# Optimization experiments

Measured on AMD Instinct MI355X. Metric: run time of the kernel, lower is better.

## Reference

```python
import jax, jax.numpy as jnp
import numpy as np

B = 512; D = 128; NL = 16; LAYERS = 4; H = 4; HD = D // H
MAX_D = 128; MAX_E = 512
N_DRUG = 25600; N_ENZ = 153600


def setup_inputs() -> dict:
    key = jax.random.key(0)
    ks = jax.random.split(key, 40)
    it = iter(range(40))
    def nrm(shape, scale=0.02):
        return jax.random.normal(ks[next(it)], shape, jnp.float32) * scale
    inp = {}
    inp["drug_k"] = jax.random.normal(ks[next(it)], (N_DRUG, D), jnp.float32)
    inp["drug_v"] = jax.random.normal(ks[next(it)], (N_DRUG, D), jnp.float32)
    inp["enzyme_k"] = jax.random.normal(ks[next(it)], (N_ENZ, D), jnp.float32)
    inp["enzyme_v"] = jax.random.normal(ks[next(it)], (N_ENZ, D), jnp.float32)
    inp["drug_batch"] = jnp.sort(jax.random.randint(ks[next(it)], (N_DRUG,), 0, B))
    inp["enzyme_batch"] = jnp.sort(jax.random.randint(ks[next(it)], (N_ENZ,), 0, B))
    inp["latents"] = nrm((1, NL, D), 1.0)
    inp["wq_d"] = nrm((LAYERS, D, D)); inp["bq_d"] = jnp.zeros((LAYERS, D), jnp.float32)
    inp["wq_e"] = nrm((LAYERS, D, D)); inp["bq_e"] = jnp.zeros((LAYERS, D), jnp.float32)
    inp["mha_d_w"] = nrm((LAYERS, 3 * D, D)); inp["mha_d_b"] = jnp.zeros((LAYERS, 3 * D), jnp.float32)
    inp["mha_d_ow"] = nrm((LAYERS, D, D)); inp["mha_d_ob"] = jnp.zeros((LAYERS, D), jnp.float32)
    inp["mha_e_w"] = nrm((LAYERS, 3 * D, D)); inp["mha_e_b"] = jnp.zeros((LAYERS, 3 * D), jnp.float32)
    inp["mha_e_ow"] = nrm((LAYERS, D, D)); inp["mha_e_ob"] = jnp.zeros((LAYERS, D), jnp.float32)
    inp["ln1_g"] = jnp.ones((LAYERS, D), jnp.float32); inp["ln1_b"] = jnp.zeros((LAYERS, D), jnp.float32)
    inp["ln2_g"] = jnp.ones((LAYERS, D), jnp.float32); inp["ln2_b"] = jnp.zeros((LAYERS, D), jnp.float32)
    inp["ffn_w1"] = nrm((LAYERS, 2 * D, D)); inp["ffn_b1"] = jnp.zeros((LAYERS, 2 * D), jnp.float32)
    inp["ffn_w2"] = nrm((LAYERS, D, 2 * D)); inp["ffn_b2"] = jnp.zeros((LAYERS, D), jnp.float32)
    inp["head_w1"] = nrm((D, D * NL)); inp["head_b1"] = jnp.zeros((D,), jnp.float32)
    inp["head_w2"] = nrm((1, D)); inp["head_b2"] = jnp.zeros((1,), jnp.float32)
    return inp


def to_dense(x, batch, max_len):
    # PyG to_dense_batch: ragged [N, D] -> padded [B, max_len, D] + bool mask
    ones = jnp.ones_like(batch)
    counts = jax.ops.segment_sum(ones, batch, num_segments=B)
    starts = jnp.concatenate([jnp.zeros((1,), counts.dtype), jnp.cumsum(counts)[:-1]])
    pos = jnp.arange(batch.shape[0]) - starts[batch]
    dense = jnp.zeros((B, max_len, x.shape[-1]), x.dtype).at[batch, pos].set(x)
    mask = jnp.zeros((B, max_len), bool).at[batch, pos].set(True)
    return dense, mask


def layer_norm(x, g, b):
    m = x.mean(-1, keepdims=True)
    v = ((x - m) ** 2).mean(-1, keepdims=True)
    return (x - m) / jnp.sqrt(v + 1e-5) * g + b


def mha(q, k, v, mask, w, b, ow, ob):
    # torch nn.MultiheadAttention (batch_first) with key_padding_mask (~mask = ignore)
    wq, wk, wv = w[:D], w[D:2 * D], w[2 * D:]
    bq, bk, bv = b[:D], b[D:2 * D], b[2 * D:]
    qh = (q @ wq.T + bq).reshape(q.shape[0], -1, H, HD)
    kh = (k @ wk.T + bk).reshape(k.shape[0], -1, H, HD)
    vh = (v @ wv.T + bv).reshape(v.shape[0], -1, H, HD)
    s = jnp.einsum('bqhd,bkhd->bhqk', qh, kh) / jnp.sqrt(jnp.float32(HD))
    s = jnp.where(mask[:, None, None, :], s, jnp.float32(-1e9))
    a = jax.nn.softmax(s, axis=-1)
    o = jnp.einsum('bhqk,bkhd->bqhd', a, vh).reshape(q.shape[0], -1, D)
    return o @ ow.T + ob


def forward_impl(drug_k, drug_v, enzyme_k, enzyme_v, latents,
                 wq_d, bq_d, wq_e, bq_e,
                 mha_d_w, mha_d_b, mha_d_ow, mha_d_ob,
                 mha_e_w, mha_e_b, mha_e_ow, mha_e_ob,
                 ln1_g, ln1_b, ln2_g, ln2_b,
                 ffn_w1, ffn_b1, ffn_w2, ffn_b2,
                 head_w1, head_b1, head_w2, head_b2,
                 drug_batch, enzyme_batch):
    dK, dM = to_dense(drug_k, drug_batch, MAX_D)
    dV, _ = to_dense(drug_v, drug_batch, MAX_D)
    eK, eM = to_dense(enzyme_k, enzyme_batch, MAX_E)
    eV, _ = to_dense(enzyme_v, enzyme_batch, MAX_E)
    lat = jnp.broadcast_to(latents, (B, NL, D))
    for l in range(LAYERS):
        nl = layer_norm(lat, ln1_g[l], ln1_b[l])
        q_d = nl @ wq_d[l].T + bq_d[l]
        q_e = nl @ wq_e[l].T + bq_e[l]
        ad = mha(q_d, dK, dV, dM, mha_d_w[l], mha_d_b[l], mha_d_ow[l], mha_d_ob[l])
        ae = mha(q_e, eK, eV, eM, mha_e_w[l], mha_e_b[l], mha_e_ow[l], mha_e_ob[l])
        lat = lat + ad + ae
        h = layer_norm(lat, ln2_g[l], ln2_b[l])
        h = jax.nn.relu(h @ ffn_w1[l].T + ffn_b1[l]) @ ffn_w2[l].T + ffn_b2[l]
        lat = lat + h
    flat = lat.reshape(B, NL * D)
    h = jax.nn.relu(flat @ head_w1.T + head_b1)
    return jax.nn.softplus(h @ head_w2.T + head_b2)[:, 0]


def reference(drug_k, drug_v, enzyme_k, enzyme_v, drug_batch, enzyme_batch, latents,
              wq_d, bq_d, wq_e, bq_e,
              mha_d_w, mha_d_b, mha_d_ow, mha_d_ob,
              mha_e_w, mha_e_b, mha_e_ow, mha_e_ob,
              ln1_g, ln1_b, ln2_g, ln2_b,
              ffn_w1, ffn_b1, ffn_w2, ffn_b2,
              head_w1, head_b1, head_w2, head_b2):
    return forward_impl(drug_k, drug_v, enzyme_k, enzyme_v, latents,
                        wq_d, bq_d, wq_e, bq_e,
                        mha_d_w, mha_d_b, mha_d_ow, mha_d_ob,
                        mha_e_w, mha_e_b, mha_e_ow, mha_e_ob,
                        ln1_g, ln1_b, ln2_g, ln2_b,
                        ffn_w1, ffn_b1, ffn_w2, ffn_b2,
                        head_w1, head_b1, head_w2, head_b2,
                        drug_batch, enzyme_batch)
```

## Files before the change

kernel.cpp:

```cpp
#include <hip/hip_runtime.h>
#include <math.h>

#define NL 16
#define DD 128

typedef __attribute__((ext_vector_type(8))) short short8;
typedef __attribute__((ext_vector_type(4))) float floatx4;

union U8 { short8 v; unsigned short s[8]; };

__device__ __forceinline__ unsigned short f2bf(float x) {
  union { float f; unsigned u; } v; v.f = x; return (unsigned short)(v.u >> 16);
}
__device__ __forceinline__ float bf2f(unsigned short s) {
  union { unsigned u; float f; } v; v.u = ((unsigned)s) << 16; return v.f;
}

__global__ void seg_kernel(const int* __restrict__ db, int nd,
                           const int* __restrict__ eb, int ne,
                           int* __restrict__ seg) {
  const int* arr = (blockIdx.x == 0) ? db : eb;
  int n = (blockIdx.x == 0) ? nd : ne;
  int* start = seg + blockIdx.x * 1024;
  int* cnt = start + 512;
  int b = threadIdx.x;
  if (b < 512) {
    int lo = 0, hi = n;
    while (lo < hi) { int mid = (lo + hi) >> 1; if (arr[mid] < b) lo = mid + 1; else hi = mid; }
    int s = lo;
    lo = s; hi = n;
    while (lo < hi) { int mid = (lo + hi) >> 1; if (arr[mid] < b + 1) lo = mid + 1; else hi = mid; }
    start[b] = s; cnt[b] = lo - s;
  }
}

__global__ void init_lat_kernel(const float* __restrict__ latents, float* __restrict__ lat) {
  int i = blockIdx.x * blockDim.x + threadIdx.x;
  ((float4*)lat)[i] = ((const float4*)latents)[i & 511];
}

__global__ void cvtw_kernel(const float* __restrict__ mw_d, const float* __restrict__ ow_d,
                            const float* __restrict__ mw_e, const float* __restrict__ ow_e,
                            const float* __restrict__ w1, const float* __restrict__ w2,
                            unsigned short* __restrict__ Wbf) {
  int l = blockIdx.x >> 7, blk = blockIdx.x & 127;
  int idx = blk * 1024 + threadIdx.x * 4;
  const float* src; int off;
  if (idx < 16384)      { src = mw_d + (size_t)l * 49152 + 32768; off = idx; }
  else if (idx < 32768) { src = ow_d + (size_t)l * 16384; off = idx - 16384; }
  else if (idx < 49152) { src = mw_e + (size_t)l * 49152 + 32768; off = idx - 32768; }
  else if (idx < 65536) { src = ow_e + (size_t)l * 16384; off = idx - 49152; }
  else if (idx < 98304) { src = w1 + (size_t)l * 32768; off = idx - 65536; }
  else                  { src = w2 + (size_t)l * 32768; off = idx - 98304; }
  float4 v = *(const float4*)(src + off);
  ushort4 o = { f2bf(v.x), f2bf(v.y), f2bf(v.z), f2bf(v.w) };
  *(ushort4*)(Wbf + (size_t)l * 131072 + idx) = o;
}

__global__ void cvth_kernel(const float* __restrict__ w1, unsigned short* __restrict__ dst) {
  int i = blockIdx.x * blockDim.x + threadIdx.x;
  float4 v = ((const float4*)w1)[i];
  ushort4 o = { f2bf(v.x), f2bf(v.y), f2bf(v.z), f2bf(v.w) };
  ((ushort4*)dst)[i] = o;
}

__global__ __launch_bounds__(256) void fold_kernel(
    const float* __restrict__ wq_d, const float* __restrict__ bq_d,
    const float* __restrict__ wq_e, const float* __restrict__ bq_e,
    const float* __restrict__ mw_d, const float* __restrict__ mb_d,
    const float* __restrict__ mw_e, const float* __restrict__ mb_e,
    float* __restrict__ Wqf, float* __restrict__ bqf) {
  __shared__ __align__(16) float sMW[2048];
  const int pb = blockIdx.x >> 3, rg = blockIdx.x & 7;
  const int l = pb >> 1, p = pb & 1;
  const float* wq = (p == 0 ? wq_d : wq_e) + (size_t)l * 16384;
  const float* bq = (p == 0 ? bq_d : bq_e) + l * 128;
  const float* mw = (p == 0 ? mw_d : mw_e) + (size_t)l * 49152;
  const float* mb = (p == 0 ? mb_d : mb_e) + l * 384;
  const float scale = 0.17677669529663687f;
  const int tid = threadIdx.x;
  {
    const float4* src = (const float4*)(mw + rg * 2048);
    ((float4*)sMW)[tid] = src[tid];
    ((float4*)sMW)[tid + 256] = src[tid + 256];
  }
  __syncthreads();
  const int j = tid & 127, ih = tid >> 7;
  float acc[8];
#pragma unroll
  for (int r = 0; r < 8; ++r) acc[r] = 0.f;
#pragma unroll 4
  for (int k = 0; k < 128; ++k) {
    float wv = wq[k * 128 + j];
#pragma unroll
    for (int r = 0; r < 8; ++r) acc[r] += sMW[(ih * 8 + r) * 128 + k] * wv;
  }
  float* W = Wqf + (size_t)pb * 16384 + (rg * 16 + ih * 8) * 128 + j;
#pragma unroll
  for (int r = 0; r < 8; ++r) W[r * 128] = acc[r] * scale;
  if (rg == 0 && tid < 128) {
    float s = 0.f;
    const float* mr = mw + tid * 128;
    for (int k = 0; k < 128; ++k) s += mr[k] * bq[k];
    bqf[pb * 128 + tid] = (s + mb[tid]) * scale;
  }
}

__global__ __launch_bounds__(256) void wt_kernel(
    const float* __restrict__ Wqf, const float* __restrict__ bqf,
    const float* __restrict__ mw_d, const float* __restrict__ mw_e,
    unsigned short* __restrict__ WtB, float* __restrict__ bt) {
  const int l = blockIdx.x >> 3, p = (blockIdx.x >> 2) & 1, h = blockIdx.x & 3;
  const float* wqf = Wqf + (size_t)(l * 2 + p) * 16384 + (h * 32) * 128;
  const float* wk  = (p == 0 ? mw_d : mw_e) + (size_t)l * 49152 + 16384 + (h * 32) * 128;
  const float* bqv = bqf + (l * 2 + p) * 128 + h * 32;
  __shared__ __align__(16) float sWq[4096];
  __shared__ __align__(16) float sWk[4096];
  __shared__ float sBq[32];
  const int tid = threadIdx.x;
  for (int i = tid; i < 1024; i += 256) {
    ((float4*)sWq)[i] = ((const float4*)wqf)[i];
    ((float4*)sWk)[i] = ((const float4*)wk)[i];
  }
  if (tid < 32) sBq[tid] = bqv[tid];
  __syncthreads();
  const int d = tid & 127, kh = tid >> 7;
  const int n = p * 512 + h * 128 + d;
  const int tn = n >> 4, m = n & 15;
  unsigned short* outl = WtB + (size_t)l * 131072;
#pragma unroll
  for (int kc = 0; kc < 4; ++kc) {
    int k0 = kh * 64 + kc * 16;
    float acc[16];
#pragma unroll
    for (int kk = 0; kk < 16; ++kk) acc[kk] = 0.f;
    for (int j = 0; j < 32; ++j) {
      float wkd = sWk[j * 128 + d];
#pragma unroll
      for (int kk = 0; kk < 16; ++kk) acc[kk] += sWq[j * 128 + k0 + kk] * wkd;
    }
#pragma unroll
    for (int kk = 0; kk < 16; ++kk) {
      int k = k0 + kk;
      int c = k >> 5, quad = (k >> 3) & 3, j8 = k & 7;
      int lane = quad * 16 + m;
      outl[(((size_t)tn * 4 + c) * 64 + lane) * 8 + j8] = f2bf(acc[kk]);
    }
  }
  if (kh == 0) {
    float a = 0.f;
    for (int j = 0; j < 32; ++j) a += sBq[j] * sWk[j * 128 + d];
    bt[l * 1024 + n] = a;
  }
}

__global__ __launch_bounds__(256) void qtilde_kernel(
    const float* __restrict__ lat,
    const float* __restrict__ lng, const float* __restrict__ lnb,
    const unsigned short* __restrict__ WtBl, const float* __restrict__ btl,
    unsigned short* __restrict__ Qt) {
  __shared__ __align__(16) unsigned short sNL[16 * 136];
  const int tid = threadIdx.x;
  const int b = blockIdx.x;
  {
    int q = tid >> 4, li = tid & 15, d0 = li * 8;
    const float* xr = lat + ((size_t)b * NL + q) * DD + d0;
    float x[8];
    *(float4*)(x) = *(const float4*)(xr);
    *(float4*)(x + 4) = *(const float4*)(xr + 4);
    float s1 = 0.f, s2 = 0.f;
#pragma unroll
    for (int j = 0; j < 8; ++j) { s1 += x[j]; s2 += x[j] * x[j]; }
#pragma unroll
    for (int o = 1; o < 16; o <<= 1) { s1 += __shfl_xor(s1, o); s2 += __shfl_xor(s2, o); }
    float mean = s1 * (1.f / 128.f);
    float var = s2 * (1.f / 128.f) - mean * mean;
    float rstd = rsqrtf(var + 1e-5f);
    float y[8];
#pragma unroll
    for (int j = 0; j < 8; ++j)
      y[j] = (x[j] - mean) * rstd * lng[d0 + j] + lnb[d0 + j];
    ushort4 o0 = { f2bf(y[0]), f2bf(y[1]), f2bf(y[2]), f2bf(y[3]) };
    ushort4 o1 = { f2bf(y[4]), f2bf(y[5]), f2bf(y[6]), f2bf(y[7]) };
    *(ushort4*)(sNL + q * 136 + d0) = o0;
    *(ushort4*)(sNL + q * 136 + d0 + 4) = o1;
  }
  __syncthreads();
  const int lane = tid & 63, w = tid >> 6, m = lane & 15, quad = lane >> 4;
  short8 aF[4];
  {
    const unsigned short* arow = sNL + m * 136 + quad * 8;
#pragma unroll
    for (int c = 0; c < 4; ++c) aF[c] = *(const short8*)(arow + c * 32);
  }
  unsigned short* qtb = Qt + (size_t)b * 16384;
#pragma unroll
  for (int t = 0; t < 16; ++t) {
    int tn = w * 16 + t;
    floatx4 acc = (floatx4){0.f, 0.f, 0.f, 0.f};
#pragma unroll
    for (int c = 0; c < 4; ++c) {
      short8 bF = *(const short8*)(WtBl + (((size_t)tn * 4 + c) * 64 + lane) * 8);
      acc = __builtin_amdgcn_mfma_f32_16x16x32_bf16(aF[c], bF, acc, 0, 0, 0);
    }
    int n = tn * 16 + m;
    float bb = btl[n];
    int p = n >> 9, h = (n >> 7) & 3, d = n & 127;
    unsigned short* op = qtb + (p * 64 + h * 16) * 128 + d;
#pragma unroll
    for (int r = 0; r < 4; ++r) op[(quad * 4 + r) * 128] = f2bf(acc[r] + bb);
  }
}

__global__ __launch_bounds__(256, 4) void attn3_kernel(
    const float* __restrict__ Kd32, const float* __restrict__ Vd32,
    const float* __restrict__ Ke32, const float* __restrict__ Ve32,
    unsigned short* __restrict__ Kd, unsigned short* __restrict__ Vd,
    unsigned short* __restrict__ Ke, unsigned short* __restrict__ Ve,
    const int* __restrict__ seg,
    const unsigned short* __restrict__ Qt, int qstride, int cvt,
    unsigned short* __restrict__ part_d, float* __restrict__ l_d,
    unsigned short* __restrict__ part_e, float* __restrict__ l_e) {
  __shared__ __align__(16) unsigned short sK[32 * 136];
  __shared__ __align__(16) unsigned short sV[128 * 40];
  __shared__ __align__(16) unsigned short sP[64 * 40];
  const int tid = threadIdx.x;
  const int bi = blockIdx.x;

  const float* Kp32; const float* Vp32;
  unsigned short* KpB; unsigned short* VpB;
  const unsigned short* qt;
  unsigned short* part; float* lpart;
  int len, st;
  if (bi < 2048) {
    int b = bi >> 2, sp = bi & 3;
    int n = seg[1536 + b]; if (n > 512) n = 512;
    int chunk = (n + 3) >> 2;
    int begin = sp * chunk;
    len = n - begin; if (len > chunk) len = chunk; if (len < 0) len = 0;
    st = seg[1024 + b] + begin;
    Kp32 = Ke32; Vp32 = Ve32; KpB = Ke; VpB = Ve;
    qt = Qt + (size_t)b * qstride + 8192;
    part = part_e + (size_t)bi * 8192;
    lpart = l_e + (size_t)bi * 64;
  } else {
    int b = bi - 2048;
    int n = seg[512 + b]; if (n > 128) n = 128;
    len = n;
    st = seg[b];
    Kp32 = Kd32; Vp32 = Vd32; KpB = Kd; VpB = Vd;
    qt = Qt + (size_t)b * qstride;
    part = part_d + (size_t)b * 8192;
    lpart = l_d + (size_t)b * 64;
  }

  const int lane = tid & 63;
  const int w = tid >> 6;
  const int m = lane & 15;
  const int quad = lane >> 4;

  short8 qA[4];
  {
    const unsigned short* qrow = qt + (size_t)(w * 16 + m) * 128 + quad * 8;
#pragma unroll
    for (int c = 0; c < 4; ++c) qA[c] = *(const short8*)(qrow + c * 32);
  }

  floatx4 oA[8];
#pragma unroll
  for (int i = 0; i < 8; ++i) oA[i] = (floatx4){0.f, 0.f, 0.f, 0.f};
  float lp[4] = {0.f, 0.f, 0.f, 0.f};

  short8 rK[2], rV[2];
  const short8 z8 = {0, 0, 0, 0, 0, 0, 0, 0};
  auto load_tile = [&](int t0) {
    int nv = len - t0; if (nv > 32) nv = 32;
    if (cvt) {
#pragma unroll
      for (int it = 0; it < 2; ++it) {
        int f = tid + it * 256;
        int tok = f >> 4, d8 = f & 15;
        if (tok < nv) {
          size_t g = (size_t)(st + t0 + tok) * 128 + d8 * 8;
          const float* s = Kp32 + g;
          float4 a = *(const float4*)s, c = *(const float4*)(s + 4);
          U8 u;
          u.s[0]=f2bf(a.x); u.s[1]=f2bf(a.y); u.s[2]=f2bf(a.z); u.s[3]=f2bf(a.w);
          u.s[4]=f2bf(c.x); u.s[5]=f2bf(c.y); u.s[6]=f2bf(c.z); u.s[7]=f2bf(c.w);
          rK[it] = u.v;
          *(short8*)(KpB + g) = u.v;
        } else rK[it] = z8;
      }
#pragma unroll
      for (int it = 0; it < 2; ++it) {
        int f = tid + it * 256;
        int tok = f >> 4, d8 = f & 15;
        if (tok < nv) {
          size_t g = (size_t)(st + t0 + tok) * 128 + d8 * 8;
          const float* s = Vp32 + g;
          float4 a = *(const float4*)s, c = *(const float4*)(s + 4);
          U8 u;
          u.s[0]=f2bf(a.x); u.s[1]=f2bf(a.y); u.s[2]=f2bf(a.z); u.s[3]=f2bf(a.w);
          u.s[4]=f2bf(c.x); u.s[5]=f2bf(c.y); u.s[6]=f2bf(c.z); u.s[7]=f2bf(c.w);
          rV[it] = u.v;
          *(short8*)(VpB + g) = u.v;
        } else rV[it] = z8;
      }
    } else {
#pragma unroll
      for (int it = 0; it < 2; ++it) {
        int f = tid + it * 256;
        int tok = f >> 4, d8 = f & 15;
        size_t g = (size_t)(st + t0 + tok) * 128 + d8 * 8;
        rK[it] = (tok < nv) ? *(const short8*)(KpB + g) : z8;
        rV[it] = (tok < nv) ? *(const short8*)(VpB + g) : z8;
      }
    }
  };
  auto store_tile = [&]() {
#pragma unroll
    for (int it = 0; it < 2; ++it) {
      int f = tid + it * 256;
      int tok = f >> 4, d8 = f & 15;
      *(short8*)(sK + tok * 136 + d8 * 8) = rK[it];
      U8 u; u.v = rV[it];
#pragma unroll
      for (int i = 0; i < 8; ++i) {
        int j = (i + d8) & 7;
        sV[(d8 * 8 + j) * 40 + tok] = u.s[j];
      }
    }
  };

  if (len > 0) load_tile(0);
  for (int t0 = 0; t0 < len; t0 += 32) {
    __syncthreads();
    store_tile();
    __syncthreads();
    if (t0 + 32 < len) load_tile(t0 + 32);
    int nv = len - t0; if (nv > 32) nv = 32;
    floatx4 sS[2];
    sS[0] = (floatx4){0.f, 0.f, 0.f, 0.f};
    sS[1] = (floatx4){0.f, 0.f, 0.f, 0.f};
#pragma unroll
    for (int g = 0; g < 2; ++g)
#pragma unroll
      for (int c = 0; c < 4; ++c) {
        short8 kB = *(const short8*)(sK + (g * 16 + m) * 136 + c * 32 + quad * 8);
        sS[g] = __builtin_amdgcn_mfma_f32_16x16x32_bf16(qA[c], kB, sS[g], 0, 0, 0);
      }
#pragma unroll
    for (int g = 0; g < 2; ++g) {
      bool valid = (g * 16 + m) < nv;
#pragma unroll
      for (int r = 0; r < 4; ++r) {
        float p = valid ? __expf(sS[g][r]) : 0.f;
        lp[r] += p;
        sP[(w * 16 + quad * 4 + r) * 40 + g * 16 + m] = f2bf(p);
      }
    }
    short8 pA = *(const short8*)(sP + (w * 16 + m) * 40 + quad * 8);
#pragma unroll
    for (int dg = 0; dg < 8; ++dg) {
      short8 vB = *(const short8*)(sV + (dg * 16 + m) * 40 + quad * 8);
      oA[dg] = __builtin_amdgcn_mfma_f32_16x16x32_bf16(pA, vB, oA[dg], 0, 0, 0);
    }
  }

#pragma unroll
  for (int r = 0; r < 4; ++r) {
    float v = lp[r];
    v += __shfl_xor(v, 1); v += __shfl_xor(v, 2);
    v += __shfl_xor(v, 4); v += __shfl_xor(v, 8);
    lp[r] = v;
  }
  if (m == 0) {
#pragma unroll
    for (int r = 0; r < 4; ++r)
      lpart[w * 16 + quad * 4 + r] = lp[r];
  }
#pragma unroll
  for (int dg = 0; dg < 8; ++dg)
#pragma unroll
    for (int r = 0; r < 4; ++r)
      part[(w * 16 + quad * 4 + r) * 128 + dg * 16 + m] = f2bf(oA[dg][r]);
}

__global__ __launch_bounds__(256) void post_kernel(
    const unsigned short* __restrict__ pd, const float* __restrict__ ldv,
    const unsigned short* __restrict__ pe, const float* __restrict__ lev,
    const unsigned short* __restrict__ Wl,
    const float* __restrict__ bv_d, const float* __restrict__ ob_d,
    const float* __restrict__ bv_e, const float* __restrict__ ob_e,
    const float* __restrict__ ln2g, const float* __restrict__ ln2b,
    const float* __restrict__ b1, const float* __restrict__ b2,
    float* __restrict__ lat,
    const float* __restrict__ lng1, const float* __restrict__ lnb1,
    const unsigned short* __restrict__ WtB_next, const float* __restrict__ bt_next,
    unsigned short* __restrict__ Qt) {
  const unsigned short* wv_d = Wl;
  const unsigned short* ow_d = Wl + 16384;
  const unsigned short* wv_e = Wl + 32768;
  const unsigned short* ow_e = Wl + 49152;
  const unsigned short* w1   = Wl + 65536;
  const unsigned short* w2   = Wl + 98304;

  __shared__ __align__(16) unsigned short sX[64 * 136];
  __shared__ __align__(16) unsigned short sVH[16 * 136];
  __shared__ __align__(16) unsigned short sF[16 * 264];
  __shared__ __align__(16) float sAcc[16 * 132];
  __shared__ float sLd[64], sLe[64];

  const int tid = threadIdx.x;
  const int b = blockIdx.x;
  const int lane = tid & 63;
  const int w = tid >> 6;
  const int m = lane & 15;
  const int quad = lane >> 4;

  if (tid < 64) {
    float v = ldv[(size_t)b * 64 + tid];
    sLd[tid] = (v > 0.f) ? 1.f / v : 0.f;
  } else if (tid < 128) {
    int r = tid - 64;
    float v = lev[((size_t)b * 4 + 0) * 64 + r] + lev[((size_t)b * 4 + 1) * 64 + r]
            + lev[((size_t)b * 4 + 2) * 64 + r] + lev[((size_t)b * 4 + 3) * 64 + r];
    sLe[r] = (v > 0.f) ? 1.f / v : 0.f;
  }
  __syncthreads();
  {
    const ushort4* src = (const ushort4*)(pd + (size_t)b * 8192);
#pragma unroll
    for (int it = 0; it < 8; ++it) {
      int f = tid + it * 256;
      int row = f >> 5, d = (f & 31) * 4;
      ushort4 u = src[f];
      float sc = sLd[row];
      ushort4 o = { f2bf(bf2f(u.x) * sc), f2bf(bf2f(u.y) * sc),
                    f2bf(bf2f(u.z) * sc), f2bf(bf2f(u.w) * sc) };
      *(ushort4*)(sX + row * 136 + d) = o;
    }
  }
  __syncthreads();
  {
    short8 aF[4];
    const unsigned short* arow = sX + (w * 16 + m) * 136 + quad * 8;
#pragma unroll
    for (int c = 0; c < 4; ++c) aF[c] = *(const short8*)(arow + c * 32);
#pragma unroll
    for (int t = 0; t < 2; ++t) {
      int n = w * 32 + t * 16 + m;
      floatx4 acc = (floatx4){0.f, 0.f, 0.f, 0.f};
      const unsigned short* brow = wv_d + n * 128 + quad * 8;
#pragma unroll
      for (int c = 0; c < 4; ++c)
        acc = __builtin_amdgcn_mfma_f32_16x16x32_bf16(aF[c], *(const short8*)(brow + c * 32), acc, 0, 0, 0);
      float bb = bv_d[n];
#pragma unroll
      for (int r = 0; r < 4; ++r) sVH[(quad * 4 + r) * 136 + n] = f2bf(acc[r] + bb);
    }
  }
  __syncthreads();
  {
    short8 aF[4];
    const unsigned short* arow = sVH + m * 136 + quad * 8;
#pragma unroll
    for (int c = 0; c < 4; ++c) aF[c] = *(const short8*)(arow + c * 32);
#pragma unroll
    for (int t = 0; t < 2; ++t) {
      int n = w * 32 + t * 16 + m;
      floatx4 acc = (floatx4){0.f, 0.f, 0.f, 0.f};
      const unsigned short* brow = ow_d + n * 128 + quad * 8;
#pragma unroll
      for (int c = 0; c < 4; ++c)
        acc = __builtin_amdgcn_mfma_f32_16x16x32_bf16(aF[c], *(const short8*)(brow + c * 32), acc, 0, 0, 0);
      float bb = ob_d[n];
#pragma unroll
      for (int r = 0; r < 4; ++r) {
        int q = quad * 4 + r;
        sAcc[q * 132 + n] = lat[(size_t)b * 2048 + q * 128 + n] + acc[r] + bb;
      }
    }
  }
  __syncthreads();
  {
    const ushort4* s0 = (const ushort4*)(pe + ((size_t)b * 4 + 0) * 8192);
    const ushort4* s1 = (const ushort4*)(pe + ((size_t)b * 4 + 1) * 8192);
    const ushort4* s2 = (const ushort4*)(pe + ((size_t)b * 4 + 2) * 8192);
    const ushort4* s3 = (const ushort4*)(pe + ((size_t)b * 4 + 3) * 8192);
#pragma unroll
    for (int it = 0; it < 8; ++it) {
      int f = tid + it * 256;
      int row = f >> 5, d = (f & 31) * 4;
      ushort4 u0 = s0[f], u1 = s1[f], u2 = s2[f], u3 = s3[f];
      float sc = sLe[row];
      ushort4 o = { f2bf((bf2f(u0.x) + bf2f(u1.x) + bf2f(u2.x) + bf2f(u3.x)) * sc),
                    f2bf((bf2f(u0.y) + bf2f(u1.y) + bf2f(u2.y) + bf2f(u3.y)) * sc),
                    f2bf((bf2f(u0.z) + bf2f(u1.z) + bf2f(u2.z) + bf2f(u3.z)) * sc),
                    f2bf((bf2f(u0.w) + bf2f(u1.w) + bf2f(u2.w) + bf2f(u3.w)) * sc) };
      *(ushort4*)(sX + row * 136 + d) = o;
    }
  }
  __syncthreads();
  {
    short8 aF[4];
    const unsigned short* arow = sX + (w * 16 + m) * 136 + quad * 8;
#pragma unroll
    for (int c = 0; c < 4; ++c) aF[c] = *(const short8*)(arow + c * 32);
#pragma unroll
    for (int t = 0; t < 2; ++t) {
      int n = w * 32 + t * 16 + m;
      floatx4 acc = (floatx4){0.f, 0.f, 0.f, 0.f};
      const unsigned short* brow = wv_e + n * 128 + quad * 8;
#pragma unroll
      for (int c = 0; c < 4; ++c)
        acc = __builtin_amdgcn_mfma_f32_16x16x32_bf16(aF[c], *(const short8*)(brow + c * 32), acc, 0, 0, 0);
      float bb = bv_e[n];
#pragma unroll
      for (int r = 0; r < 4; ++r) sVH[(quad * 4 + r) * 136 + n] = f2bf(acc[r] + bb);
    }
  }
  __syncthreads();
  {
    short8 aF[4];
    const unsigned short* arow = sVH + m * 136 + quad * 8;
#pragma unroll
    for (int c = 0; c < 4; ++c) aF[c] = *(const short8*)(arow + c * 32);
#pragma unroll
    for (int t = 0; t < 2; ++t) {
      int n = w * 32 + t * 16 + m;
      floatx4 acc = (floatx4){0.f, 0.f, 0.f, 0.f};
      const unsigned short* brow = ow_e + n * 128 + quad * 8;
#pragma unroll
      for (int c = 0; c < 4; ++c)
        acc = __builtin_amdgcn_mfma_f32_16x16x32_bf16(aF[c], *(const short8*)(brow + c * 32), acc, 0, 0, 0);
      float bb = ob_e[n];
#pragma unroll
      for (int r = 0; r < 4; ++r) {
        int q = quad * 4 + r;
        sAcc[q * 132 + n] += acc[r] + bb;
      }
    }
  }
  __syncthreads();
  {
    int q = tid >> 4, li = tid & 15, d0 = li * 8;
    float x[8];
#pragma unroll
    for (int j = 0; j < 8; ++j) x[j] = sAcc[q * 132 + d0 + j];
    float s1 = 0.f, s2 = 0.f;
#pragma unroll
    for (int j = 0; j < 8; ++j) { s1 += x[j]; s2 += x[j] * x[j]; }
#pragma unroll
    for (int o = 1; o < 16; o <<= 1) { s1 += __shfl_xor(s1, o); s2 += __shfl_xor(s2, o); }
    float mean = s1 * (1.f / 128.f);
    float var = s2 * (1.f / 128.f) - mean * mean;
    float rstd = rsqrtf(var + 1e-5f);
    float y[8];
#pragma unroll
    for (int j = 0; j < 8; ++j)
      y[j] = (x[j] - mean) * rstd * ln2g[d0 + j] + ln2b[d0 + j];
    ushort4 o0 = { f2bf(y[0]), f2bf(y[1]), f2bf(y[2]), f2bf(y[3]) };
    ushort4 o1 = { f2bf(y[4]), f2bf(y[5]), f2bf(y[6]), f2bf(y[7]) };
    *(ushort4*)(sX + q * 136 + d0) = o0;
    *(ushort4*)(sX + q * 136 + d0 + 4) = o1;
  }
  __syncthreads();
  {
    short8 aF[4];
    const unsigned short* arow = sX + m * 136 + quad * 8;
#pragma unroll
    for (int c = 0; c < 4; ++c) aF[c] = *(const short8*)(arow + c * 32);
#pragma unroll
    for (int t = 0; t < 4; ++t) {
      int n = w * 64 + t * 16 + m;
      floatx4 acc = (floatx4){0.f, 0.f, 0.f, 0.f};
      const unsigned short* brow = w1 + n * 128 + quad * 8;
#pragma unroll
      for (int c = 0; c < 4; ++c)
        acc = __builtin_amdgcn_mfma_f32_16x16x32_bf16(aF[c], *(const short8*)(brow + c * 32), acc, 0, 0, 0);
      float bb = b1[n];
#pragma unroll
      for (int r = 0; r < 4; ++r)
        sF[(quad * 4 + r) * 264 + n] = f2bf(fmaxf(acc[r] + bb, 0.f));
    }
  }
  __syncthreads();
  {
    short8 aF[8];
    const unsigned short* arow = sF + m * 264 + quad * 8;
#pragma unroll
    for (int c = 0; c < 8; ++c) aF[c] = *(const short8*)(arow + c * 32);
#pragma unroll
    for (int t = 0; t < 2; ++t) {
      int n = w * 32 + t * 16 + m;
      floatx4 acc = (floatx4){0.f, 0.f, 0.f, 0.f};
      const unsigned short* brow = w2 + n * 256 + quad * 8;
#pragma unroll
      for (int c = 0; c < 8; ++c)
        acc = __builtin_amdgcn_mfma_f32_16x16x32_bf16(aF[c], *(const short8*)(brow + c * 32), acc, 0, 0, 0);
      float bb = b2[n];
#pragma unroll
      for (int r = 0; r < 4; ++r) {
        int q = quad * 4 + r;
        float fin = sAcc[q * 132 + n] + acc[r] + bb;
        lat[(size_t)b * 2048 + q * 128 + n] = fin;
        sAcc[q * 132 + n] = fin;
      }
    }
  }
  if (WtB_next) {
    __syncthreads();
    {
      int q = tid >> 4, li = tid & 15, d0 = li * 8;
      float x[8];
#pragma unroll
      for (int j = 0; j < 8; ++j) x[j] = sAcc[q * 132 + d0 + j];
      float s1 = 0.f, s2 = 0.f;
#pragma unroll
      for (int j = 0; j < 8; ++j) { s1 += x[j]; s2 += x[j] * x[j]; }
#pragma unroll
      for (int o = 1; o < 16; o <<= 1) { s1 += __shfl_xor(s1, o); s2 += __shfl_xor(s2, o); }
      float mean = s1 * (1.f / 128.f);
      float var = s2 * (1.f / 128.f) - mean * mean;
      float rstd = rsqrtf(var + 1e-5f);
      float y[8];
#pragma unroll
      for (int j = 0; j < 8; ++j)
        y[j] = (x[j] - mean) * rstd * lng1[d0 + j] + lnb1[d0 + j];
      ushort4 o0 = { f2bf(y[0]), f2bf(y[1]), f2bf(y[2]), f2bf(y[3]) };
      ushort4 o1 = { f2bf(y[4]), f2bf(y[5]), f2bf(y[6]), f2bf(y[7]) };
      *(ushort4*)(sX + q * 136 + d0) = o0;
      *(ushort4*)(sX + q * 136 + d0 + 4) = o1;
    }
    __syncthreads();
    short8 aF[4];
    const unsigned short* arow = sX + m * 136 + quad * 8;
#pragma unroll
    for (int c = 0; c < 4; ++c) aF[c] = *(const short8*)(arow + c * 32);
    unsigned short* qtb = Qt + (size_t)b * 16384;
#pragma unroll
    for (int t = 0; t < 16; ++t) {
      int tn = w * 16 + t;
      floatx4 acc = (floatx4){0.f, 0.f, 0.f, 0.f};
#pragma unroll
      for (int c = 0; c < 4; ++c) {
        short8 bF = *(const short8*)(WtB_next + (((size_t)tn * 4 + c) * 64 + lane) * 8);
        acc = __builtin_amdgcn_mfma_f32_16x16x32_bf16(aF[c], bF, acc, 0, 0, 0);
      }
      int n = tn * 16 + m;
      float bb = bt_next[n];
      int p = n >> 9, h = (n >> 7) & 3, d = n & 127;
      unsigned short* op = qtb + (p * 64 + h * 16) * 128 + d;
#pragma unroll
      for (int r = 0; r < 4; ++r) op[(quad * 4 + r) * 128] = f2bf(acc[r] + bb);
    }
  }
}

__global__ __launch_bounds__(256) void head_kernel(
    const float* __restrict__ lat, const unsigned short* __restrict__ w1b,
    const float* __restrict__ b1, const float* __restrict__ w2,
    const float* __restrict__ b2, float* __restrict__ out) {
  __shared__ __align__(16) unsigned short sA[16 * 2056];
  __shared__ float sW[4][16];
  const int tid = threadIdx.x;
  const int b0 = blockIdx.x * 16;
  for (int i = tid; i < 8192; i += 256) {
    int bb = i >> 9, c4 = i & 511;
    float4 v = ((const float4*)(lat + (size_t)(b0 + bb) * 2048))[c4];
    ushort4 u = { f2bf(v.x), f2bf(v.y), f2bf(v.z), f2bf(v.w) };
    *(ushort4*)(sA + bb * 2056 + c4 * 4) = u;
  }
  __syncthreads();
  const int lane = tid & 63, w = tid >> 6, m = lane & 15, quad = lane >> 4;
  float s[4] = {0.f, 0.f, 0.f, 0.f};
#pragma unroll
  for (int t = 0; t < 2; ++t) {
    int nt = w * 2 + t;
    int o = nt * 16 + m;
    floatx4 acc = (floatx4){0.f, 0.f, 0.f, 0.f};
    const unsigned short* brow = w1b + (size_t)o * 2048 + quad * 8;
    const unsigned short* arow = sA + m * 2056 + quad * 8;
    for (int c = 0; c < 64; ++c) {
      short8 aF = *(const short8*)(arow + c * 32);
      short8 bF = *(const short8*)(brow + c * 32);
      acc = __builtin_amdgcn_mfma_f32_16x16x32_bf16(aF, bF, acc, 0, 0, 0);
    }
    float w2v = w2[o];
    float b1v = b1[o];
#pragma unroll
    for (int r = 0; r < 4; ++r)
      s[r] += fmaxf(acc[r] + b1v, 0.f) * w2v;
  }
#pragma unroll
  for (int r = 0; r < 4; ++r) {
    float v = s[r];
    v += __shfl_xor(v, 1); v += __shfl_xor(v, 2);
    v += __shfl_xor(v, 4); v += __shfl_xor(v, 8);
    s[r] = v;
  }
  if (m == 0) {
#pragma unroll
    for (int r = 0; r < 4; ++r) sW[w][quad * 4 + r] = s[r];
  }
  __syncthreads();
  if (tid < 16) {
    float x = sW[0][tid] + sW[1][tid] + sW[2][tid] + sW[3][tid] + b2[0];
    out[b0 + tid] = (x > 20.f) ? x : log1pf(__expf(x));
  }
}

extern "C" void kernel_launch(void* const* d_in, const int* in_sizes, int n_in,
                              void* d_out, int out_size, void* d_ws, size_t ws_size,
                              hipStream_t stream) {
  const float* drug_k  = (const float*)d_in[0];
  const float* drug_v  = (const float*)d_in[1];
  const float* enz_k   = (const float*)d_in[2];
  const float* enz_v   = (const float*)d_in[3];
  const int*   drug_b  = (const int*)d_in[4];
  const int*   enz_b   = (const int*)d_in[5];
  const float* latents = (const float*)d_in[6];
  const float* wq_d    = (const float*)d_in[7];
  const float* bq_d    = (const float*)d_in[8];
  const float* wq_e    = (const float*)d_in[9];
  const float* bq_e    = (const float*)d_in[10];
  const float* mha_d_w = (const float*)d_in[11];
  const float* mha_d_b = (const float*)d_in[12];
  const float* mha_d_ow= (const float*)d_in[13];
  const float* mha_d_ob= (const float*)d_in[14];
  const float* mha_e_w = (const float*)d_in[15];
  const float* mha_e_b = (const float*)d_in[16];
  const float* mha_e_ow= (const float*)d_in[17];
  const float* mha_e_ob= (const float*)d_in[18];
  const float* ln1_g   = (const float*)d_in[19];
  const float* ln1_b   = (const float*)d_in[20];
  const float* ln2_g   = (const float*)d_in[21];
  const float* ln2_b   = (const float*)d_in[22];
  const float* ffn_w1  = (const float*)d_in[23];
  const float* ffn_b1  = (const float*)d_in[24];
  const float* ffn_w2  = (const float*)d_in[25];
  const float* ffn_b2  = (const float*)d_in[26];
  const float* head_w1 = (const float*)d_in[27];
  const float* head_b1 = (const float*)d_in[28];
  const float* head_w2 = (const float*)d_in[29];
  const float* head_b2 = (const float*)d_in[30];
  float* out = (float*)d_out;

  const int n_dk = in_sizes[0];
  const int n_ek = in_sizes[2];

  int* seg = (int*)d_ws;
  float* fws = (float*)d_ws;
  float* Wqf = fws + 2048;
  float* bqf = Wqf + 131072;
  float* lat = bqf + 1024;
  float* l_d = lat + 1048576;
  float* l_e = l_d + 32768;
  unsigned short* Qt     = (unsigned short*)(l_e + 131072);
  unsigned short* part_d = Qt + 8388608;
  unsigned short* part_e = part_d + 4194304;
  unsigned short* Kd_bf  = part_e + 16777216;
  unsigned short* Vd_bf  = Kd_bf + n_dk;
  unsigned short* Ke_bf  = Vd_bf + n_dk;
  unsigned short* Ve_bf  = Ke_bf + n_ek;
  unsigned short* Wbf    = Ve_bf + n_ek;
  unsigned short* WtB    = Wbf + 524288;
  float* bt              = (float*)(WtB + 524288);
  unsigned short* w1h    = (unsigned short*)(bt + 4096);

  seg_kernel<<<2, 512, 0, stream>>>(drug_b, in_sizes[4], enz_b, in_sizes[5], seg);
  init_lat_kernel<<<1024, 256, 0, stream>>>(latents, lat);
  fold_kernel<<<64, 256, 0, stream>>>(wq_d, bq_d, wq_e, bq_e,
                                      mha_d_w, mha_d_b, mha_e_w, mha_e_b, Wqf, bqf);
  wt_kernel<<<32, 256, 0, stream>>>(Wqf, bqf, mha_d_w, mha_e_w, WtB, bt);
  cvtw_kernel<<<512, 256, 0, stream>>>(mha_d_w, mha_d_ow, mha_e_w, mha_e_ow,
                                       ffn_w1, ffn_w2, Wbf);
  cvth_kernel<<<256, 256, 0, stream>>>(head_w1, w1h);
  qtilde_kernel<<<1, 256, 0, stream>>>(lat, ln1_g, ln1_b, WtB, bt, Qt);
  for (int l = 0; l < 4; ++l) {
    attn3_kernel<<<2560, 256, 0, stream>>>(drug_k, drug_v, enz_k, enz_v,
        Kd_bf, Vd_bf, Ke_bf, Ve_bf, seg,
        Qt, (l == 0) ? 0 : 16384, (l == 0) ? 1 : 0,
        part_d, l_d, part_e, l_e);
    const unsigned short* wtn = (l < 3) ? (WtB + (size_t)(l + 1) * 131072) : nullptr;
    const float* btn = (l < 3) ? (bt + (l + 1) * 1024) : nullptr;
    post_kernel<<<512, 256, 0, stream>>>(part_d, l_d, part_e, l_e,
        Wbf + (size_t)l * 131072,
        mha_d_b + l * 384 + 256, mha_d_ob + l * 128,
        mha_e_b + l * 384 + 256, mha_e_ob + l * 128,
        ln2_g + l * 128, ln2_b + l * 128,
        ffn_b1 + l * 256, ffn_b2 + l * 128,
        lat,
        ln1_g + (l + 1 < 4 ? (l + 1) * 128 : 0), ln1_b + (l + 1 < 4 ? (l + 1) * 128 : 0),
        wtn, btn, Qt);
  }
  head_kernel<<<32, 256, 0, stream>>>(lat, w1h, head_b1, head_w2, head_b2, out);
}
```

Baseline: 645.6 us.

## Move bf16 K/V conversion to extra blocks and coalesce output stores via LDS

In the first layer, the scattered bf16 write-back of converted K/V tiles inside the attention blocks is replaced by 2048 extra blocks that run a flat grid-stride fp32-to-bf16 conversion of all four K/V arrays. The attention partial outputs and the next-layer Q-tilde projection in post_kernel are now staged through shared memory so global stores become coalesced ushort4 rows instead of strided 2-byte writes. This adds extra __syncthreads and a larger grid in layer 0, which compete with the attention work. The conversion also covers every token, including ones the attention path clips at the max length.

```diff
diff --git a/kernel.cpp b/kernel.cpp
--- a/kernel.cpp
+++ b/kernel.cpp
@@ -218,17 +218,37 @@
     unsigned short* __restrict__ Kd, unsigned short* __restrict__ Vd,
     unsigned short* __restrict__ Ke, unsigned short* __restrict__ Ve,
     const int* __restrict__ seg,
-    const unsigned short* __restrict__ Qt, int qstride, int cvt,
+    const unsigned short* __restrict__ Qt, int qstride, int f32in,
+    int ncvt, int ndk4, int nek4,
     unsigned short* __restrict__ part_d, float* __restrict__ l_d,
     unsigned short* __restrict__ part_e, float* __restrict__ l_e) {
-  __shared__ __align__(16) unsigned short sK[32 * 136];
-  __shared__ __align__(16) unsigned short sV[128 * 40];
-  __shared__ __align__(16) unsigned short sP[64 * 40];
+  __shared__ __align__(16) unsigned short smem[12032];
+  unsigned short* sK = smem;
+  unsigned short* sV = smem + 4352;
+  unsigned short* sP = smem + 9472;
+  unsigned short* sO = smem;
   const int tid = threadIdx.x;
   const int bi = blockIdx.x;
 
+  if (bi >= 2560) {
+    int idx0 = (bi - 2560) * 256 + tid;
+    int stride = ncvt * 256;
+    int tot = 2 * ndk4 + 2 * nek4;
+    for (int i = idx0; i < tot; i += stride) {
+      const float* s; unsigned short* o; int r;
+      if (i < ndk4)               { s = Kd32; o = Kd; r = i; }
+      else if (i < 2 * ndk4)      { s = Vd32; o = Vd; r = i - ndk4; }
+      else if (i < 2 * ndk4 + nek4) { s = Ke32; o = Ke; r = i - 2 * ndk4; }
+      else                        { s = Ve32; o = Ve; r = i - 2 * ndk4 - nek4; }
+      float4 v = ((const float4*)s)[r];
+      ushort4 u = { f2bf(v.x), f2bf(v.y), f2bf(v.z), f2bf(v.w) };
+      ((ushort4*)o)[r] = u;
+    }
+    return;
+  }
+
   const float* Kp32; const float* Vp32;
-  unsigned short* KpB; unsigned short* VpB;
+  const unsigned short* KpB; const unsigned short* VpB;
   const unsigned short* qt;
   unsigned short* part; float* lpart;
   int len, st;
@@ -275,7 +295,7 @@
   const short8 z8 = {0, 0, 0, 0, 0, 0, 0, 0};
   auto load_tile = [&](int t0) {
     int nv = len - t0; if (nv > 32) nv = 32;
-    if (cvt) {
+    if (f32in) {
 #pragma unroll
       for (int it = 0; it < 2; ++it) {
         int f = tid + it * 256;
@@ -288,7 +308,6 @@
           u.s[0]=f2bf(a.x); u.s[1]=f2bf(a.y); u.s[2]=f2bf(a.z); u.s[3]=f2bf(a.w);
           u.s[4]=f2bf(c.x); u.s[5]=f2bf(c.y); u.s[6]=f2bf(c.z); u.s[7]=f2bf(c.w);
           rK[it] = u.v;
-          *(short8*)(KpB + g) = u.v;
         } else rK[it] = z8;
       }
 #pragma unroll
@@ -303,7 +322,6 @@
           u.s[0]=f2bf(a.x); u.s[1]=f2bf(a.y); u.s[2]=f2bf(a.z); u.s[3]=f2bf(a.w);
           u.s[4]=f2bf(c.x); u.s[5]=f2bf(c.y); u.s[6]=f2bf(c.z); u.s[7]=f2bf(c.w);
           rV[it] = u.v;
-          *(short8*)(VpB + g) = u.v;
         } else rV[it] = z8;
       }
     } else {
@@ -379,11 +397,19 @@
     for (int r = 0; r < 4; ++r)
       lpart[w * 16 + quad * 4 + r] = lp[r];
   }
+  __syncthreads();
 #pragma unroll
   for (int dg = 0; dg < 8; ++dg)
 #pragma unroll
     for (int r = 0; r < 4; ++r)
-      part[(w * 16 + quad * 4 + r) * 128 + dg * 16 + m] = f2bf(oA[dg][r]);
+      sO[(w * 16 + quad * 4 + r) * 132 + dg * 16 + m] = f2bf(oA[dg][r]);
+  __syncthreads();
+#pragma unroll
+  for (int it = 0; it < 8; ++it) {
+    int f = tid + it * 256;
+    int row = f >> 5, c4 = f & 31;
+    *(ushort4*)(part + row * 128 + c4 * 4) = *(const ushort4*)(sO + row * 132 + c4 * 4);
+  }
 }
 
 __global__ __launch_bounds__(256) void post_kernel(
@@ -635,25 +661,41 @@
     }
     __syncthreads();
     short8 aF[4];
-    const unsigned short* arow = sX + m * 136 + quad * 8;
-#pragma unroll
-    for (int c = 0; c < 4; ++c) aF[c] = *(const short8*)(arow + c * 32);
+    {
+      const unsigned short* arow = sX + m * 136 + quad * 8;
+#pragma unroll
+      for (int c = 0; c < 4; ++c) aF[c] = *(const short8*)(arow + c * 32);
+    }
+    __syncthreads();
     unsigned short* qtb = Qt + (size_t)b * 16384;
-#pragma unroll
-    for (int t = 0; t < 16; ++t) {
-      int tn = w * 16 + t;
-      floatx4 acc = (floatx4){0.f, 0.f, 0.f, 0.f};
-#pragma unroll
-      for (int c = 0; c < 4; ++c) {
-        short8 bF = *(const short8*)(WtB_next + (((size_t)tn * 4 + c) * 64 + lane) * 8);
-        acc = __builtin_amdgcn_mfma_f32_16x16x32_bf16(aF[c], bF, acc, 0, 0, 0);
-      }
-      int n = tn * 16 + m;
-      float bb = bt_next[n];
-      int p = n >> 9, h = (n >> 7) & 3, d = n & 127;
-      unsigned short* op = qtb + (p * 64 + h * 16) * 128 + d;
-#pragma unroll
-      for (int r = 0; r < 4; ++r) op[(quad * 4 + r) * 128] = f2bf(acc[r] + bb);
+    for (int half = 0; half < 2; ++half) {
+      if (half) __syncthreads();
+#pragma unroll
+      for (int t8 = 0; t8 < 8; ++t8) {
+        int t = half * 8 + t8;
+        int tn = w * 16 + t;
+        floatx4 acc = (floatx4){0.f, 0.f, 0.f, 0.f};
+#pragma unroll
+        for (int c = 0; c < 4; ++c) {
+          short8 bF = *(const short8*)(WtB_next + (((size_t)tn * 4 + c) * 64 + lane) * 8);
+          acc = __builtin_amdgcn_mfma_f32_16x16x32_bf16(aF[c], bF, acc, 0, 0, 0);
+        }
+        int n = tn * 16 + m;
+        float bb = bt_next[n];
+#pragma unroll
+        for (int r = 0; r < 4; ++r)
+          sX[(w * 16 + quad * 4 + r) * 132 + t8 * 16 + m] = f2bf(acc[r] + bb);
+      }
+      __syncthreads();
+#pragma unroll
+      for (int it = 0; it < 8; ++it) {
+        int f = tid + it * 256;
+        int lr = f >> 5, c4 = f & 31;
+        int ww = lr >> 4;
+        int p = ww >> 1, hh = (ww * 2 + half) & 3;
+        int qrow = p * 64 + hh * 16 + (lr & 15);
+        *(ushort4*)(qtb + qrow * 128 + c4 * 4) = *(const ushort4*)(sX + lr * 132 + c4 * 4);
+      }
     }
   }
 }
@@ -779,9 +821,11 @@
   cvth_kernel<<<256, 256, 0, stream>>>(head_w1, w1h);
   qtilde_kernel<<<1, 256, 0, stream>>>(lat, ln1_g, ln1_b, WtB, bt, Qt);
   for (int l = 0; l < 4; ++l) {
-    attn3_kernel<<<2560, 256, 0, stream>>>(drug_k, drug_v, enz_k, enz_v,
+    int ncvt = (l == 0) ? 2048 : 0;
+    attn3_kernel<<<2560 + ncvt, 256, 0, stream>>>(drug_k, drug_v, enz_k, enz_v,
         Kd_bf, Vd_bf, Ke_bf, Ve_bf, seg,
         Qt, (l == 0) ? 0 : 16384, (l == 0) ? 1 : 0,
+        ncvt, n_dk / 4, n_ek / 4,
         part_d, l_d, part_e, l_e);
     const unsigned short* wtn = (l < 3) ? (WtB + (size_t)(l + 1) * 131072) : nullptr;
     const float* btn = (l < 3) ? (bt + (l + 1) * 1024) : nullptr;
```

Measured after the change: 810.2 us. 1.25x slower.

## Read fp32 K/V directly each layer and split Q projection into its own kernel

Applied to the files above, without the earlier changes.

Drops the bf16 K/V cache that layer 0 wrote and later layers read. Every layer now loads fp32 K/V and converts it to bf16 on the fly, which roughly doubles K/V read traffic on layers 1-3 but removes the bf16 write on layer 0. The next-layer Q projection moves out of post_kernel into a separate qtilde_kernel launched each layer over 512 blocks, which adds a launch per layer. Attention output partials are now staged through shared memory so global stores are coalesced.

```diff
diff --git a/kernel.cpp b/kernel.cpp
--- a/kernel.cpp
+++ b/kernel.cpp
@@ -213,22 +213,21 @@
 }
 
 __global__ __launch_bounds__(256, 4) void attn3_kernel(
-    const float* __restrict__ Kd32, const float* __restrict__ Vd32,
-    const float* __restrict__ Ke32, const float* __restrict__ Ve32,
-    unsigned short* __restrict__ Kd, unsigned short* __restrict__ Vd,
-    unsigned short* __restrict__ Ke, unsigned short* __restrict__ Ve,
+    const float* __restrict__ Kd, const float* __restrict__ Vd,
+    const float* __restrict__ Ke, const float* __restrict__ Ve,
     const int* __restrict__ seg,
-    const unsigned short* __restrict__ Qt, int qstride, int cvt,
+    const unsigned short* __restrict__ Qt,
     unsigned short* __restrict__ part_d, float* __restrict__ l_d,
     unsigned short* __restrict__ part_e, float* __restrict__ l_e) {
-  __shared__ __align__(16) unsigned short sK[32 * 136];
-  __shared__ __align__(16) unsigned short sV[128 * 40];
-  __shared__ __align__(16) unsigned short sP[64 * 40];
+  __shared__ __align__(16) unsigned short smem[12032];
+  unsigned short* sK = smem;
+  unsigned short* sV = smem + 4352;
+  unsigned short* sP = smem + 9472;
+  unsigned short* sO = smem;
   const int tid = threadIdx.x;
   const int bi = blockIdx.x;
 
-  const float* Kp32; const float* Vp32;
-  unsigned short* KpB; unsigned short* VpB;
+  const float* Kp; const float* Vp;
   const unsigned short* qt;
   unsigned short* part; float* lpart;
   int len, st;
@@ -239,8 +238,8 @@
     int begin = sp * chunk;
     len = n - begin; if (len > chunk) len = chunk; if (len < 0) len = 0;
     st = seg[1024 + b] + begin;
-    Kp32 = Ke32; Vp32 = Ve32; KpB = Ke; VpB = Ve;
-    qt = Qt + (size_t)b * qstride + 8192;
+    Kp = Ke; Vp = Ve;
+    qt = Qt + (size_t)b * 16384 + 8192;
     part = part_e + (size_t)bi * 8192;
     lpart = l_e + (size_t)bi * 64;
   } else {
@@ -248,8 +247,8 @@
     int n = seg[512 + b]; if (n > 128) n = 128;
     len = n;
     st = seg[b];
-    Kp32 = Kd32; Vp32 = Vd32; KpB = Kd; VpB = Vd;
-    qt = Qt + (size_t)b * qstride;
+    Kp = Kd; Vp = Vd;
+    qt = Qt + (size_t)b * 16384;
     part = part_d + (size_t)b * 8192;
     lpart = l_d + (size_t)b * 64;
   }
@@ -275,46 +274,33 @@
   const short8 z8 = {0, 0, 0, 0, 0, 0, 0, 0};
   auto load_tile = [&](int t0) {
     int nv = len - t0; if (nv > 32) nv = 32;
-    if (cvt) {
-#pragma unroll
-      for (int it = 0; it < 2; ++it) {
-        int f = tid + it * 256;
-        int tok = f >> 4, d8 = f & 15;
-        if (tok < nv) {
-          size_t g = (size_t)(st + t0 + tok) * 128 + d8 * 8;
-          const float* s = Kp32 + g;
-          float4 a = *(const float4*)s, c = *(const float4*)(s + 4);
-          U8 u;
-          u.s[0]=f2bf(a.x); u.s[1]=f2bf(a.y); u.s[2]=f2bf(a.z); u.s[3]=f2bf(a.w);
-          u.s[4]=f2bf(c.x); u.s[5]=f2bf(c.y); u.s[6]=f2bf(c.z); u.s[7]=f2bf(c.w);
-          rK[it] = u.v;
-          *(short8*)(KpB + g) = u.v;
-        } else rK[it] = z8;
-      }
-#pragma unroll
-      for (int it = 0; it < 2; ++it) {
-        int f = tid + it * 256;
-        int tok = f >> 4, d8 = f & 15;
-        if (tok < nv) {
-          size_t g = (size_t)(st + t0 + tok) * 128 + d8 * 8;
-          const float* s = Vp32 + g;
-          float4 a = *(const float4*)s, c = *(const float4*)(s + 4);
-          U8 u;
-          u.s[0]=f2bf(a.x); u.s[1]=f2bf(a.y); u.s[2]=f2bf(a.z); u.s[3]=f2bf(a.w);
-          u.s[4]=f2bf(c.x); u.s[5]=f2bf(c.y); u.s[6]=f2bf(c.z); u.s[7]=f2bf(c.w);
-          rV[it] = u.v;
-          *(short8*)(VpB + g) = u.v;
-        } else rV[it] = z8;
-      }
-    } else {
-#pragma unroll
-      for (int it = 0; it < 2; ++it) {
-        int f = tid + it * 256;
-        int tok = f >> 4, d8 = f & 15;
+#pragma unroll
+    for (int it = 0; it < 2; ++it) {
+      int f = tid + it * 256;
+      int tok = f >> 4, d8 = f & 15;
+      if (tok < nv) {
         size_t g = (size_t)(st + t0 + tok) * 128 + d8 * 8;
-        rK[it] = (tok < nv) ? *(const short8*)(KpB + g) : z8;
-        rV[it] = (tok < nv) ? *(const short8*)(VpB + g) : z8;
-      }
+        const float* s = Kp + g;
+        float4 a = *(const float4*)s, c = *(const float4*)(s + 4);
+        U8 u;
+        u.s[0]=f2bf(a.x); u.s[1]=f2bf(a.y); u.s[2]=f2bf(a.z); u.s[3]=f2bf(a.w);
+        u.s[4]=f2bf(c.x); u.s[5]=f2bf(c.y); u.s[6]=f2bf(c.z); u.s[7]=f2bf(c.w);
+        rK[it] = u.v;
+      } else rK[it] = z8;
+    }
+#pragma unroll
+    for (int it = 0; it < 2; ++it) {
+      int f = tid + it * 256;
+      int tok = f >> 4, d8 = f & 15;
+      if (tok < nv) {
+        size_t g = (size_t)(st + t0 + tok) * 128 + d8 * 8;
+        const float* s = Vp + g;
+        float4 a = *(const float4*)s, c = *(const float4*)(s + 4);
+        U8 u;
+        u.s[0]=f2bf(a.x); u.s[1]=f2bf(a.y); u.s[2]=f2bf(a.z); u.s[3]=f2bf(a.w);
+        u.s[4]=f2bf(c.x); u.s[5]=f2bf(c.y); u.s[6]=f2bf(c.z); u.s[7]=f2bf(c.w);
+        rV[it] = u.v;
+      } else rV[it] = z8;
     }
   };
   auto store_tile = [&]() {
@@ -379,11 +365,19 @@
     for (int r = 0; r < 4; ++r)
       lpart[w * 16 + quad * 4 + r] = lp[r];
   }
+  __syncthreads();
 #pragma unroll
   for (int dg = 0; dg < 8; ++dg)
 #pragma unroll
     for (int r = 0; r < 4; ++r)
-      part[(w * 16 + quad * 4 + r) * 128 + dg * 16 + m] = f2bf(oA[dg][r]);
+      sO[(w * 16 + quad * 4 + r) * 132 + dg * 16 + m] = f2bf(oA[dg][r]);
+  __syncthreads();
+#pragma unroll
+  for (int it = 0; it < 8; ++it) {
+    int f = tid + it * 256;
+    int row = f >> 5, c4 = f & 31;
+    *(ushort4*)(part + row * 128 + c4 * 4) = *(const ushort4*)(sO + row * 132 + c4 * 4);
+  }
 }
 
 __global__ __launch_bounds__(256) void post_kernel(
@@ -394,10 +388,7 @@
     const float* __restrict__ bv_e, const float* __restrict__ ob_e,
     const float* __restrict__ ln2g, const float* __restrict__ ln2b,
     const float* __restrict__ b1, const float* __restrict__ b2,
-    float* __restrict__ lat,
-    const float* __restrict__ lng1, const float* __restrict__ lnb1,
-    const unsigned short* __restrict__ WtB_next, const float* __restrict__ bt_next,
-    unsigned short* __restrict__ Qt) {
+    float* __restrict__ lat) {
   const unsigned short* wv_d = Wl;
   const unsigned short* ow_d = Wl + 16384;
   const unsigned short* wv_e = Wl + 32768;
@@ -603,57 +594,8 @@
 #pragma unroll
       for (int r = 0; r < 4; ++r) {
         int q = quad * 4 + r;
-        float fin = sAcc[q * 132 + n] + acc[r] + bb;
-        lat[(size_t)b * 2048 + q * 128 + n] = fin;
-        sAcc[q * 132 + n] = fin;
+        lat[(size_t)b * 2048 + q * 128 + n] = sAcc[q * 132 + n] + acc[r] + bb;
       }
-    }
-  }
-  if (WtB_next) {
-    __syncthreads();
-    {
-      int q = tid >> 4, li = tid & 15, d0 = li * 8;
-      float x[8];
-#pragma unroll
-      for (int j = 0; j < 8; ++j) x[j] = sAcc[q * 132 + d0 + j];
-      float s1 = 0.f, s2 = 0.f;
-#pragma unroll
-      for (int j = 0; j < 8; ++j) { s1 += x[j]; s2 += x[j] * x[j]; }
-#pragma unroll
-      for (int o = 1; o < 16; o <<= 1) { s1 += __shfl_xor(s1, o); s2 += __shfl_xor(s2, o); }
-      float mean = s1 * (1.f / 128.f);
-      float var = s2 * (1.f / 128.f) - mean * mean;
-      float rstd = rsqrtf(var + 1e-5f);
-      float y[8];
-#pragma unroll
-      for (int j = 0; j < 8; ++j)
-        y[j] = (x[j] - mean) * rstd * lng1[d0 + j] + lnb1[d0 + j];
-      ushort4 o0 = { f2bf(y[0]), f2bf(y[1]), f2bf(y[2]), f2bf(y[3]) };
-      ushort4 o1 = { f2bf(y[4]), f2bf(y[5]), f2bf(y[6]), f2bf(y[7]) };
-      *(ushort4*)(sX + q * 136 + d0) = o0;
-      *(ushort4*)(sX + q * 136 + d0 + 4) = o1;
-    }
-    __syncthreads();
-    short8 aF[4];
-    const unsigned short* arow = sX + m * 136 + quad * 8;
-#pragma unroll
-    for (int c = 0; c < 4; ++c) aF[c] = *(const short8*)(arow + c * 32);
-    unsigned short* qtb = Qt + (size_t)b * 16384;
-#pragma unroll
-    for (int t = 0; t < 16; ++t) {
-      int tn = w * 16 + t;
-      floatx4 acc = (floatx4){0.f, 0.f, 0.f, 0.f};
-#pragma unroll
-      for (int c = 0; c < 4; ++c) {
-        short8 bF = *(const short8*)(WtB_next + (((size_t)tn * 4 + c) * 64 + lane) * 8);
-        acc = __builtin_amdgcn_mfma_f32_16x16x32_bf16(aF[c], bF, acc, 0, 0, 0);
-      }
-      int n = tn * 16 + m;
-      float bb = bt_next[n];
-      int p = n >> 9, h = (n >> 7) & 3, d = n & 127;
-      unsigned short* op = qtb + (p * 64 + h * 16) * 128 + d;
-#pragma unroll
-      for (int r = 0; r < 4; ++r) op[(quad * 4 + r) * 128] = f2bf(acc[r] + bb);
     }
   }
 }
@@ -747,9 +689,6 @@
   const float* head_b2 = (const float*)d_in[30];
   float* out = (float*)d_out;
 
-  const int n_dk = in_sizes[0];
-  const int n_ek = in_sizes[2];
-
   int* seg = (int*)d_ws;
   float* fws = (float*)d_ws;
   float* Wqf = fws + 2048;
@@ -760,11 +699,7 @@
   unsigned short* Qt     = (unsigned short*)(l_e + 131072);
   unsigned short* part_d = Qt + 8388608;
   unsigned short* part_e = part_d + 4194304;
-  unsigned short* Kd_bf  = part_e + 16777216;
-  unsigned short* Vd_bf  = Kd_bf + n_dk;
-  unsigned short* Ke_bf  = Vd_bf + n_dk;
-  unsigned short* Ve_bf  = Ke_bf + n_ek;
-  unsigned short* Wbf    = Ve_bf + n_ek;
+  unsigned short* Wbf    = part_e + 16777216;
   unsigned short* WtB    = Wbf + 524288;
   float* bt              = (float*)(WtB + 524288);
   unsigned short* w1h    = (unsigned short*)(bt + 4096);
@@ -777,23 +712,18 @@
   cvtw_kernel<<<512, 256, 0, stream>>>(mha_d_w, mha_d_ow, mha_e_w, mha_e_ow,
                                        ffn_w1, ffn_w2, Wbf);
   cvth_kernel<<<256, 256, 0, stream>>>(head_w1, w1h);
-  qtilde_kernel<<<1, 256, 0, stream>>>(lat, ln1_g, ln1_b, WtB, bt, Qt);
   for (int l = 0; l < 4; ++l) {
-    attn3_kernel<<<2560, 256, 0, stream>>>(drug_k, drug_v, enz_k, enz_v,
-        Kd_bf, Vd_bf, Ke_bf, Ve_bf, seg,
-        Qt, (l == 0) ? 0 : 16384, (l == 0) ? 1 : 0,
-        part_d, l_d, part_e, l_e);
-    const unsigned short* wtn = (l < 3) ? (WtB + (size_t)(l + 1) * 131072) : nullptr;
-    const float* btn = (l < 3) ? (bt + (l + 1) * 1024) : nullptr;
+    qtilde_kernel<<<512, 256, 0, stream>>>(lat, ln1_g + l * 128, ln1_b + l * 128,
+        WtB + (size_t)l * 131072, bt + l * 1024, Qt);
+    attn3_kernel<<<2560, 256, 0, stream>>>(drug_k, drug_v, enz_k, enz_v, seg,
+        Qt, part_d, l_d, part_e, l_e);
     post_kernel<<<512, 256, 0, stream>>>(part_d, l_d, part_e, l_e,
         Wbf + (size_t)l * 131072,
         mha_d_b + l * 384 + 256, mha_d_ob + l * 128,
         mha_e_b + l * 384 + 256, mha_e_ob + l * 128,
         ln2_g + l * 128, ln2_b + l * 128,
         ffn_b1 + l * 256, ffn_b2 + l * 128,
-        lat,
-        ln1_g + (l + 1 < 4 ? (l + 1) * 128 : 0), ln1_b + (l + 1 < 4 ? (l + 1) * 128 : 0),
-        wtn, btn, Qt);
+        lat);
   }
   head_kernel<<<32, 256, 0, stream>>>(lat, w1h, head_b1, head_w2, head_b2, out);
 }
```

Measured after the change: 708.6 us. 1.1x slower.
